# Kernel tuning notes

Measured on AMD Instinct MI355X. Metric: run time of the kernel, lower is better.

## Reference

```python
import jax, jax.numpy as jnp
import numpy as np

B, L, DIM, H, HD = 1, 2048, 2048, 16, 128  # head_dim = DIM // H; RoPE pairs = HD // 2


def setup_inputs() -> dict:
    key = jax.random.key(0)
    ks = jax.random.split(key, 6)
    x = jax.random.normal(ks[0], (B, L, DIM), dtype=jnp.float32)
    pe = jax.random.normal(ks[1], (1, 1, L, HD // 2, 2, 2), dtype=jnp.float32)
    qkv_w = jax.random.normal(ks[2], (3 * DIM, DIM), dtype=jnp.float32) * 0.02
    q_scale = jnp.ones((HD,), dtype=jnp.float32)
    k_scale = jnp.ones((HD,), dtype=jnp.float32)
    proj_w = jax.random.normal(ks[3], (DIM, DIM), dtype=jnp.float32) * 0.02
    proj_b = jnp.zeros((DIM,), dtype=jnp.float32)
    return {"x": x, "pe": pe, "qkv_w": qkv_w, "q_scale": q_scale,
            "k_scale": k_scale, "proj_w": proj_w, "proj_b": proj_b}


def _rmsnorm(t, scale):
    # per-head-dim RMSNorm, eps=1e-6, computed in fp32 (inputs already fp32)
    rrms = jax.lax.rsqrt(jnp.mean(t * t, axis=-1, keepdims=True) + 1e-6)
    return t * rrms * scale


def _apply_rope(q, k, pe):
    def rot(t):
        t_ = t.reshape(*t.shape[:-1], -1, 1, 2)  # [B,H,L,HD/2,1,2]
        out = pe[..., 0] * t_[..., 0] + pe[..., 1] * t_[..., 1]  # [B,H,L,HD/2,2]
        return out.reshape(t.shape)
    return rot(q), rot(k)


def reference(x, pe, qkv_w, q_scale, k_scale, proj_w, proj_b):
    b, l, _ = x.shape
    qkv = jnp.einsum('bld,ed->ble', x, qkv_w)  # [B, L, 3*DIM]
    qkv = qkv.reshape(b, l, 3, H, HD)
    # 'B L (K H D) -> K B H L D'
    qkv = jnp.transpose(qkv, (2, 0, 3, 1, 4))
    q, k, v = qkv[0], qkv[1], qkv[2]  # each [B, H, L, HD]
    q = _rmsnorm(q, q_scale)
    k = _rmsnorm(k, k_scale)
    q, k = _apply_rope(q, k, pe)
    scale = 1.0 / jnp.sqrt(jnp.asarray(HD, dtype=q.dtype))
    scores = jnp.einsum('bhqd,bhkd->bhqk', q, k) * scale
    attn = jax.nn.softmax(scores, axis=-1)
    out = jnp.einsum('bhqk,bhkd->bhqd', attn, v)  # [B, H, L, HD]
    out = jnp.transpose(out, (0, 2, 1, 3)).reshape(b, l, H * HD)  # 'B H L D -> B L (H D)'
    return jnp.einsum('bld,ed->ble', out, proj_w) + proj_b
```

## Files before the change

kernel.cpp:

```cpp
#include <hip/hip_runtime.h>
#include <hip/hip_bf16.h>
#include <math.h>

#define L_SEQ 2048
#define DIM   2048
#define NH    16
#define HD    128
#define TDIM  6144

typedef __attribute__((ext_vector_type(8))) short short8;
typedef __attribute__((ext_vector_type(4))) float f32x4;
typedef __attribute__((ext_vector_type(4))) unsigned int u32x4;

__device__ __forceinline__ void gl_lds16(const void* g, void* l) {
  __builtin_amdgcn_global_load_lds(
      (const __attribute__((address_space(1))) unsigned int*)g,
      (__attribute__((address_space(3))) unsigned int*)l, 16, 0, 0);
}

__device__ __forceinline__ short bf16bits(float x) {
  __hip_bfloat16 h = __float2bfloat16(x);
  return *(short*)&h;
}

__device__ __forceinline__ float bits2f(short s) {
  unsigned int u = ((unsigned int)(unsigned short)s) << 16;
  return __uint_as_float(u);
}

__device__ __forceinline__ unsigned int pack_bf16(float a, float b) {
  __hip_bfloat162 h = __float22bfloat162_rn(make_float2(a, b));
  return *(unsigned int*)&h;
}

__global__ __launch_bounds__(256)
void cast2_bf16(const float* __restrict__ a, __hip_bfloat16* __restrict__ oa,
                const float* __restrict__ b, __hip_bfloat16* __restrict__ ob) {
  int i = (blockIdx.x * 256 + threadIdx.x) * 8;
  const float* src;
  __hip_bfloat16* dst;
  int off;
  if (i < DIM * DIM) { src = a; dst = oa; off = i; }
  else               { src = b; dst = ob; off = i - DIM * DIM; }
  float4 v0 = *(const float4*)(src + off);
  float4 v1 = *(const float4*)(src + off + 4);
  short8 o;
  o[0] = bf16bits(v0.x); o[1] = bf16bits(v0.y); o[2] = bf16bits(v0.z); o[3] = bf16bits(v0.w);
  o[4] = bf16bits(v1.x); o[5] = bf16bits(v1.y); o[6] = bf16bits(v1.z); o[7] = bf16bits(v1.w);
  *(short8*)(dst + off) = o;
}

__global__ __launch_bounds__(256)
void cast_bf16(const float* __restrict__ in, __hip_bfloat16* __restrict__ out, int n) {
  int i = (blockIdx.x * 256 + threadIdx.x) * 8;
  if (i >= n) return;
  float4 a = *(const float4*)(in + i);
  float4 b = *(const float4*)(in + i + 4);
  short8 o;
  o[0] = bf16bits(a.x); o[1] = bf16bits(a.y); o[2] = bf16bits(a.z); o[3] = bf16bits(a.w);
  o[4] = bf16bits(b.x); o[5] = bf16bits(b.y); o[6] = bf16bits(b.z); o[7] = bf16bits(b.w);
  *(short8*)(out + i) = o;
}

template<int OUT_MODE>
__global__ __launch_bounds__(256)
void gemm_mfma(const __hip_bfloat16* __restrict__ A, const __hip_bfloat16* __restrict__ B,
               const float* __restrict__ bias, void* __restrict__ Cout,
               int M, int N, int K) {
  const int n0 = blockIdx.x * 128, m0 = blockIdx.y * 128;
  const int t = threadIdx.x, lane = t & 63, w = t >> 6;
  const int l15 = lane & 15, quad = lane >> 4;
  const int wm = (w & 1) * 64, wn = (w >> 1) * 64;

  __shared__ __align__(16) __hip_bfloat16 As[128 * 32];
  __shared__ __align__(16) __hip_bfloat16 Bs[128 * 32];

  f32x4 acc[4][4];
#pragma unroll
  for (int mt = 0; mt < 4; ++mt)
#pragma unroll
    for (int nt = 0; nt < 4; ++nt) acc[mt][nt] = (f32x4){0.f, 0.f, 0.f, 0.f};

  const int arow  = lane >> 2;
  const int acol8 = (lane & 3) * 8;
  const __hip_bfloat16* Ab = A + (size_t)(m0 + w * 16 + arow) * K + acol8;
  const __hip_bfloat16* Bb = B + (size_t)(n0 + w * 16 + arow) * K + acol8;
  __hip_bfloat16* As_base = As + (size_t)(w * 16) * 32;
  __hip_bfloat16* Bs_base = Bs + (size_t)(w * 16) * 32;

  for (int kb = 0; kb < K; kb += 32) {
    gl_lds16(Ab + kb,                As_base);
    gl_lds16(Ab + kb + (size_t)64*K, As_base + 64 * 32);
    gl_lds16(Bb + kb,                Bs_base);
    gl_lds16(Bb + kb + (size_t)64*K, Bs_base + 64 * 32);
    __syncthreads();

    short8 am[4], bn[4];
#pragma unroll
    for (int mt = 0; mt < 4; ++mt)
      am[mt] = *(const short8*)&As[(size_t)(wm + mt*16 + l15) * 32 + quad * 8];
#pragma unroll
    for (int nt = 0; nt < 4; ++nt)
      bn[nt] = *(const short8*)&Bs[(size_t)(wn + nt*16 + l15) * 32 + quad * 8];
#pragma unroll
    for (int mt = 0; mt < 4; ++mt)
#pragma unroll
      for (int nt = 0; nt < 4; ++nt)
        acc[mt][nt] = __builtin_amdgcn_mfma_f32_16x16x32_bf16(am[mt], bn[nt], acc[mt][nt], 0, 0, 0);
    __syncthreads();
  }

#pragma unroll
  for (int mt = 0; mt < 4; ++mt) {
#pragma unroll
    for (int nt = 0; nt < 4; ++nt) {
      int col = n0 + wn + nt * 16 + l15;
#pragma unroll
      for (int r = 0; r < 4; ++r) {
        int row = m0 + wm + mt * 16 + quad * 4 + r;
        if (OUT_MODE == 0) {
          ((__hip_bfloat16*)Cout)[(size_t)row * N + col] = __float2bfloat16(acc[mt][nt][r]);
        } else {
          ((float*)Cout)[(size_t)row * N + col] = acc[mt][nt][r] + bias[col];
        }
      }
    }
  }
}

__global__ __launch_bounds__(128)
void norm_rope(const __hip_bfloat16* __restrict__ qkv_b, const float* __restrict__ pe,
               const float* __restrict__ q_scale, const float* __restrict__ k_scale,
               __hip_bfloat16* __restrict__ Qb, __hip_bfloat16* __restrict__ Kb) {
  const int l  = blockIdx.x;
  const int hh = blockIdx.y;
  const int qk_sel = hh >> 4;
  const int h  = hh & 15;
  const int d  = threadIdx.x;
  const __hip_bfloat16* row = qkv_b + (size_t)l * TDIM + qk_sel * DIM + h * HD;
  const float* scale = qk_sel ? k_scale : q_scale;

  float v  = __bfloat162float(row[d]);
  float sq = v * v;
#pragma unroll
  for (int o = 32; o > 0; o >>= 1) sq += __shfl_xor(sq, o);
  __shared__ float wsum[2];
  if ((d & 63) == 0) wsum[d >> 6] = sq;
  __syncthreads();
  float rrms = rsqrtf((wsum[0] + wsum[1]) * (1.f / 128.f) + 1e-6f);
  __shared__ float nb[128];
  nb[d] = v * rrms * scale[d];
  __syncthreads();
  int i = d >> 1, c = d & 1;
  const float* p = pe + ((size_t)(l * 64 + i) * 2 + c) * 2;
  float res = p[0] * nb[2*i] + p[1] * nb[2*i + 1];
  size_t o_idx = ((size_t)h * L_SEQ + l) * HD + d;
  if (qk_sel == 0) Qb[o_idx] = __float2bfloat16(res * 0.08838834764831845f);
  else             Kb[o_idx] = __float2bfloat16(res);
}

__global__ __launch_bounds__(256)
void v_transpose(const __hip_bfloat16* __restrict__ qkv_b, __hip_bfloat16* __restrict__ Vt) {
  const int l0 = blockIdx.x * 64;
  const int h  = blockIdx.y;
  const int t  = threadIdx.x;
  __shared__ __align__(16) __hip_bfloat16 T[128][72];
#pragma unroll
  for (int it = 0; it < 4; ++it) {
    int idx = t + it * 256;
    int row = idx >> 4;
    int c8  = (idx & 15) * 8;
    short8 v = *(const short8*)&qkv_b[(size_t)(l0 + row) * TDIM + 2 * DIM + h * HD + c8];
#pragma unroll
    for (int j = 0; j < 8; ++j) *(short*)&T[c8 + j][row] = v[j];
  }
  __syncthreads();
#pragma unroll
  for (int it = 0; it < 4; ++it) {
    int idx = t + it * 256;
    int d = idx >> 3, c8 = (idx & 7) * 8;
    *(short8*)(Vt + ((size_t)h * HD + d) * L_SEQ + l0 + c8) = *(const short8*)&T[d][c8];
  }
}

__global__ __launch_bounds__(256, 4)
void attn_mfma(const __hip_bfloat16* __restrict__ Qb,
               const __hip_bfloat16* __restrict__ Kb,
               const __hip_bfloat16* __restrict__ Vt,
               __hip_bfloat16* __restrict__ Opart, float2* __restrict__ ml) {
  const int q0 = blockIdx.x * 64;
  const int h  = blockIdx.y;
  const int z  = blockIdx.z;
  const int t  = threadIdx.x;
  const int lane = t & 63, w = t >> 6;
  const int l15 = lane & 15, quad = lane >> 4;
  const int sw = l15 & 7;

  __shared__ __align__(16) __hip_bfloat16 Ks[64 * 128];
  __shared__ __align__(16) __hip_bfloat16 Vs[128 * 64];

  const __hip_bfloat16* kbase = Kb + (size_t)h * L_SEQ * HD;
  const __hip_bfloat16* vbase = Vt + (size_t)h * HD * L_SEQ;

  short8 aq[4];
  {
    const __hip_bfloat16* qbase = Qb + ((size_t)h * L_SEQ + q0 + w * 16 + l15) * HD;
#pragma unroll
    for (int ks = 0; ks < 4; ++ks)
      aq[ks] = *(const short8*)(qbase + ks * 32 + quad * 8);
  }

  f32x4 o[8];
#pragma unroll
  for (int n2 = 0; n2 < 8; ++n2) o[n2] = (f32x4){0.f, 0.f, 0.f, 0.f};
  float m_run = -1e30f, l_run = 0.f;

  for (int kt = 0; kt < 16; ++kt) {
    const int k0 = z * (L_SEQ / 2) + kt * 64;
#pragma unroll
    for (int i = 0; i < 4; ++i) {
      int krow = w * 16 + i * 4 + (lane >> 4);
      int kch  = (lane & 15) ^ (krow & 7);
      gl_lds16(kbase + (size_t)(k0 + krow) * HD + kch * 8,
               &Ks[(w * 16 + i * 4) * 128]);
    }
#pragma unroll
    for (int i = 0; i < 4; ++i) {
      int vrow = w * 32 + i * 8 + (lane >> 3);
      int vch  = (lane & 7) ^ (vrow & 7);
      gl_lds16(vbase + (size_t)vrow * L_SEQ + k0 + vch * 8,
               &Vs[(w * 32 + i * 8) * 64]);
    }
    __syncthreads();

    f32x4 s[4];
#pragma unroll
    for (int nt = 0; nt < 4; ++nt) s[nt] = (f32x4){0.f, 0.f, 0.f, 0.f};
#pragma unroll
    for (int ks = 0; ks < 4; ++ks) {
      short8 bk[4];
#pragma unroll
      for (int nt = 0; nt < 4; ++nt)
        bk[nt] = *(const short8*)&Ks[(nt * 16 + l15) * 128 + ((ks * 4 + quad) ^ sw) * 8];
#pragma unroll
      for (int nt = 0; nt < 4; ++nt)
        s[nt] = __builtin_amdgcn_mfma_f32_16x16x32_bf16(bk[nt], aq[ks], s[nt], 0, 0, 0);
    }

    float mx0 = fmaxf(fmaxf(s[0][0], s[0][1]), fmaxf(s[0][2], s[0][3]));
    float mx1 = fmaxf(fmaxf(s[1][0], s[1][1]), fmaxf(s[1][2], s[1][3]));
    float mx2 = fmaxf(fmaxf(s[2][0], s[2][1]), fmaxf(s[2][2], s[2][3]));
    float mx3 = fmaxf(fmaxf(s[3][0], s[3][1]), fmaxf(s[3][2], s[3][3]));
    float rm = fmaxf(fmaxf(mx0, mx1), fmaxf(mx2, mx3));
    rm = fmaxf(rm, __shfl_xor(rm, 16));
    rm = fmaxf(rm, __shfl_xor(rm, 32));
    float mnew = fmaxf(m_run, rm);
    float alpha = __expf(m_run - mnew);
    m_run = mnew;

    float sum = 0.f;
#pragma unroll
    for (int nt = 0; nt < 4; ++nt)
#pragma unroll
      for (int r = 0; r < 4; ++r) {
        float p = __expf(s[nt][r] - mnew);
        s[nt][r] = p;
        sum += p;
      }
    sum += __shfl_xor(sum, 16);
    sum += __shfl_xor(sum, 32);
    l_run = l_run * alpha + sum;

    float alpha_r[4];
#pragma unroll
    for (int r = 0; r < 4; ++r) alpha_r[r] = __shfl(alpha, quad * 4 + r);
#pragma unroll
    for (int n2 = 0; n2 < 8; ++n2)
#pragma unroll
      for (int r = 0; r < 4; ++r) o[n2][r] *= alpha_r[r];

    unsigned int pk[4][2];
#pragma unroll
    for (int nt = 0; nt < 4; ++nt) {
      pk[nt][0] = pack_bf16(s[nt][0], s[nt][1]);
      pk[nt][1] = pack_bf16(s[nt][2], s[nt][3]);
    }
    short8 ap[2];
#pragma unroll
    for (int ks2 = 0; ks2 < 2; ++ks2) {
      u32x4 a32;
#pragma unroll
      for (int jp = 0; jp < 4; ++jp) {
        int quad_src = (quad & 1) * 2 + (jp >> 1);
        int src = (quad_src << 4) | l15;
        int rp = jp & 1;
        unsigned int v0 = __shfl((int)pk[2 * ks2 + 0][rp], src);
        unsigned int v1 = __shfl((int)pk[2 * ks2 + 1][rp], src);
        a32[jp] = (quad >> 1) ? v1 : v0;
      }
      ap[ks2] = *(short8*)&a32;
    }

#pragma unroll
    for (int ks2 = 0; ks2 < 2; ++ks2)
#pragma unroll
      for (int n2 = 0; n2 < 8; ++n2) {
        short8 bv = *(const short8*)&Vs[(n2 * 16 + l15) * 64 + ((ks2 * 4 + quad) ^ sw) * 8];
        o[n2] = __builtin_amdgcn_mfma_f32_16x16x32_bf16(ap[ks2], bv, o[n2], 0, 0, 0);
      }

    __syncthreads();
  }

  const size_t rb = (size_t)(z * NH + h) * L_SEQ + q0 + w * 16;
  float linv[4];
#pragma unroll
  for (int r = 0; r < 4; ++r) linv[r] = 1.f / __shfl(l_run, quad * 4 + r);
#pragma unroll
  for (int r = 0; r < 4; ++r) {
    size_t row = rb + quad * 4 + r;
#pragma unroll
    for (int n2 = 0; n2 < 8; ++n2)
      Opart[row * HD + n2 * 16 + l15] = __float2bfloat16(o[n2][r] * linv[r]);
  }
  if (quad == 0) ml[rb + l15] = make_float2(m_run, l_run);
}

__global__ __launch_bounds__(256)
void attn_combine(const __hip_bfloat16* __restrict__ Opart,
                  const float2* __restrict__ ml,
                  __hip_bfloat16* __restrict__ out) {
  const int h  = blockIdx.y;
  const int q  = blockIdx.x * 16 + (threadIdx.x >> 4);
  const int d8 = (threadIdx.x & 15) * 8;
  const size_t i0 = (size_t)h * L_SEQ + q;
  const size_t i1 = (size_t)(NH + h) * L_SEQ + q;
  float2 a = ml[i0], b = ml[i1];
  float M  = fmaxf(a.x, b.x);
  float w1 = __expf(a.x - M) * a.y;
  float w2 = __expf(b.x - M) * b.y;
  float inv = 1.f / (w1 + w2);
  w1 *= inv; w2 *= inv;
  short8 o1 = *(const short8*)&Opart[i0 * HD + d8];
  short8 o2 = *(const short8*)&Opart[i1 * HD + d8];
  short8 r;
#pragma unroll
  for (int j = 0; j < 8; ++j)
    r[j] = bf16bits(w1 * bits2f(o1[j]) + w2 * bits2f(o2[j]));
  *(short8*)&out[(size_t)q * DIM + h * HD + d8] = r;
}

extern "C" void kernel_launch(void* const* d_in, const int* in_sizes, int n_in,
                              void* d_out, int out_size, void* d_ws, size_t ws_size,
                              hipStream_t stream) {
  const float* x       = (const float*)d_in[0];
  const float* pe      = (const float*)d_in[1];
  const float* qkv_w   = (const float*)d_in[2];
  const float* q_scale = (const float*)d_in[3];
  const float* k_scale = (const float*)d_in[4];
  const float* proj_w  = (const float*)d_in[5];
  const float* proj_b  = (const float*)d_in[6];
  float* out = (float*)d_out;

  char* base = (char*)d_ws;
  __hip_bfloat16* wb       = (__hip_bfloat16*)base;
  __hip_bfloat16* qkv_b    = (__hip_bfloat16*)(base + 25165824);
  __hip_bfloat16* xb       = (__hip_bfloat16*)(base + 50331648);
  __hip_bfloat16* Qb       = (__hip_bfloat16*)base;
  __hip_bfloat16* Kb       = (__hip_bfloat16*)(base + 8388608);
  __hip_bfloat16* Vt       = (__hip_bfloat16*)(base + 16777216);
  __hip_bfloat16* pwb      = (__hip_bfloat16*)(base + 25165824);
  __hip_bfloat16* Opart    = (__hip_bfloat16*)(base + 33554432);
  float2*         ml       = (float2*)(base + 50331648);
  __hip_bfloat16* attn_out = (__hip_bfloat16*)base;

  cast2_bf16<<<dim3((DIM * DIM + TDIM * DIM) / (256 * 8)), 256, 0, stream>>>(
      x, xb, qkv_w, wb);

  gemm_mfma<0><<<dim3(TDIM / 128, L_SEQ / 128), 256, 0, stream>>>(
      xb, wb, nullptr, qkv_b, L_SEQ, TDIM, DIM);

  norm_rope<<<dim3(L_SEQ, 2 * NH), 128, 0, stream>>>(qkv_b, pe, q_scale, k_scale, Qb, Kb);
  v_transpose<<<dim3(L_SEQ / 64, NH), 256, 0, stream>>>(qkv_b, Vt);

  cast_bf16<<<dim3(DIM * DIM / (256 * 8)), 256, 0, stream>>>(proj_w, pwb, DIM * DIM);

  attn_mfma<<<dim3(L_SEQ / 64, NH, 2), 256, 0, stream>>>(Qb, Kb, Vt, Opart, ml);
  attn_combine<<<dim3(L_SEQ / 16, NH), 256, 0, stream>>>(Opart, ml, attn_out);

  gemm_mfma<1><<<dim3(DIM / 128, DIM / 128), 256, 0, stream>>>(
      attn_out, pwb, proj_b, out, L_SEQ, DIM, DIM);
}
```

Measured before the change: 343.0 us.

## Fuse RMSNorm, RoPE and V transpose into the QKV GEMM epilogue

The QKV GEMM epilogue now stages each 128x128 output tile in shared memory. For Q and K column tiles it applies per-head RMSNorm, RoPE and the softmax scale, then writes the head-major Qb and Kb directly. For V tiles it writes the transposed Vt layout. This drops the qkv_b intermediate round trip through global memory and two kernel launches, at the cost of a larger shared-memory footprint and a heavier GEMM epilogue. Workspace offsets are reshuffled so the buffers do not alias.

```diff
diff --git a/kernel.cpp b/kernel.cpp
--- a/kernel.cpp
+++ b/kernel.cpp
@@ -62,18 +62,22 @@
   *(short8*)(out + i) = o;
 }
 
-template<int OUT_MODE>
 __global__ __launch_bounds__(256)
-void gemm_mfma(const __hip_bfloat16* __restrict__ A, const __hip_bfloat16* __restrict__ B,
-               const float* __restrict__ bias, void* __restrict__ Cout,
-               int M, int N, int K) {
-  const int n0 = blockIdx.x * 128, m0 = blockIdx.y * 128;
+void gemm_qkv_fused(const __hip_bfloat16* __restrict__ A, const __hip_bfloat16* __restrict__ B,
+                    const float* __restrict__ q_scale, const float* __restrict__ k_scale,
+                    const float* __restrict__ pe,
+                    __hip_bfloat16* __restrict__ Qb, __hip_bfloat16* __restrict__ Kb,
+                    __hip_bfloat16* __restrict__ Vt) {
+  const int K = DIM;
+  const int bx = blockIdx.x;
+  const int n0 = bx * 128, m0 = blockIdx.y * 128;
   const int t = threadIdx.x, lane = t & 63, w = t >> 6;
   const int l15 = lane & 15, quad = lane >> 4;
   const int wm = (w & 1) * 64, wn = (w >> 1) * 64;
 
-  __shared__ __align__(16) __hip_bfloat16 As[128 * 32];
-  __shared__ __align__(16) __hip_bfloat16 Bs[128 * 32];
+  __shared__ __align__(16) char smem[128 * 136 * 2];
+  __hip_bfloat16* As = (__hip_bfloat16*)smem;
+  __hip_bfloat16* Bs = As + 128 * 32;
 
   f32x4 acc[4][4];
 #pragma unroll
@@ -110,77 +114,142 @@
     __syncthreads();
   }
 
-#pragma unroll
-  for (int mt = 0; mt < 4; ++mt) {
+  __hip_bfloat16* T = (__hip_bfloat16*)smem;
+
+  if (bx < 32) {
+    const float* scale = (bx < 16) ? q_scale : k_scale;
+    const float qmul = (bx < 16) ? 0.08838834764831845f : 1.0f;
+    __hip_bfloat16* dst = (bx < 16) ? Qb : Kb;
+    const int h = bx & 15;
+
+#pragma unroll
+    for (int mt = 0; mt < 4; ++mt)
+#pragma unroll
+      for (int nt = 0; nt < 4; ++nt) {
+        int d = wn + nt * 16 + l15;
+#pragma unroll
+        for (int r = 0; r < 4; ++r)
+          T[(wm + mt * 16 + quad * 4 + r) * 136 + d] = __float2bfloat16(acc[mt][nt][r]);
+      }
+    __syncthreads();
+
+    const int row  = t >> 1;
+    const int half = t & 1;
+    const __hip_bfloat16* Trow = T + row * 136 + half * 64;
+
+    float ss = 0.f;
+#pragma unroll
+    for (int c8 = 0; c8 < 64; c8 += 8) {
+      short8 v8 = *(const short8*)(Trow + c8);
+#pragma unroll
+      for (int j = 0; j < 8; ++j) { float f = bits2f(v8[j]); ss += f * f; }
+    }
+    ss += __shfl_xor(ss, 1);
+    const float rrms = rsqrtf(ss * (1.f / 128.f) + 1e-6f);
+
+    const int l = m0 + row;
+    const float* perow = pe + (size_t)l * 256 + half * 128;
+    __hip_bfloat16* drow = dst + ((size_t)h * L_SEQ + l) * HD + half * 64;
+
+#pragma unroll
+    for (int c8 = 0; c8 < 64; c8 += 8) {
+      short8 v8 = *(const short8*)(Trow + c8);
+      float f[8];
+#pragma unroll
+      for (int j = 0; j < 8; ++j)
+        f[j] = bits2f(v8[j]) * rrms * scale[half * 64 + c8 + j];
+      short8 o;
+#pragma unroll
+      for (int p = 0; p < 4; ++p) {
+        float4 pp = *(const float4*)(perow + c8 * 2 + p * 4);
+        float e = f[2 * p], od = f[2 * p + 1];
+        o[2 * p]     = bf16bits((pp.x * e + pp.y * od) * qmul);
+        o[2 * p + 1] = bf16bits((pp.z * e + pp.w * od) * qmul);
+      }
+      *(short8*)(drow + c8) = o;
+    }
+  } else {
+    const int h = bx - 32;
+#pragma unroll
+    for (int mt = 0; mt < 4; ++mt)
+#pragma unroll
+      for (int nt = 0; nt < 4; ++nt) {
+        int d = wn + nt * 16 + l15;
+#pragma unroll
+        for (int r = 0; r < 4; ++r) {
+          int l_local = wm + mt * 16 + quad * 4 + r;
+          T[d * 136 + l_local] = __float2bfloat16(acc[mt][nt][r]);
+        }
+      }
+    __syncthreads();
+#pragma unroll
+    for (int it = 0; it < 8; ++it) {
+      int idx = t + it * 256;
+      int d = idx >> 4, c8 = (idx & 15) * 8;
+      short8 v = *(const short8*)&T[d * 136 + c8];
+      *(short8*)&Vt[((size_t)h * HD + d) * L_SEQ + m0 + c8] = v;
+    }
+  }
+}
+
+__global__ __launch_bounds__(256)
+void gemm_proj(const __hip_bfloat16* __restrict__ A, const __hip_bfloat16* __restrict__ B,
+               const float* __restrict__ bias, float* __restrict__ C,
+               int M, int N, int K) {
+  const int n0 = blockIdx.x * 128, m0 = blockIdx.y * 128;
+  const int t = threadIdx.x, lane = t & 63, w = t >> 6;
+  const int l15 = lane & 15, quad = lane >> 4;
+  const int wm = (w & 1) * 64, wn = (w >> 1) * 64;
+
+  __shared__ __align__(16) __hip_bfloat16 As[128 * 32];
+  __shared__ __align__(16) __hip_bfloat16 Bs[128 * 32];
+
+  f32x4 acc[4][4];
+#pragma unroll
+  for (int mt = 0; mt < 4; ++mt)
+#pragma unroll
+    for (int nt = 0; nt < 4; ++nt) acc[mt][nt] = (f32x4){0.f, 0.f, 0.f, 0.f};
+
+  const int arow  = lane >> 2;
+  const int acol8 = (lane & 3) * 8;
+  const __hip_bfloat16* Ab = A + (size_t)(m0 + w * 16 + arow) * K + acol8;
+  const __hip_bfloat16* Bb = B + (size_t)(n0 + w * 16 + arow) * K + acol8;
+  __hip_bfloat16* As_base = As + (size_t)(w * 16) * 32;
+  __hip_bfloat16* Bs_base = Bs + (size_t)(w * 16) * 32;
+
+  for (int kb = 0; kb < K; kb += 32) {
+    gl_lds16(Ab + kb,                As_base);
+    gl_lds16(Ab + kb + (size_t)64*K, As_base + 64 * 32);
+    gl_lds16(Bb + kb,                Bs_base);
+    gl_lds16(Bb + kb + (size_t)64*K, Bs_base + 64 * 32);
+    __syncthreads();
+
+    short8 am[4], bn[4];
+#pragma unroll
+    for (int mt = 0; mt < 4; ++mt)
+      am[mt] = *(const short8*)&As[(size_t)(wm + mt*16 + l15) * 32 + quad * 8];
+#pragma unroll
+    for (int nt = 0; nt < 4; ++nt)
+      bn[nt] = *(const short8*)&Bs[(size_t)(wn + nt*16 + l15) * 32 + quad * 8];
+#pragma unroll
+    for (int mt = 0; mt < 4; ++mt)
+#pragma unroll
+      for (int nt = 0; nt < 4; ++nt)
+        acc[mt][nt] = __builtin_amdgcn_mfma_f32_16x16x32_bf16(am[mt], bn[nt], acc[mt][nt], 0, 0, 0);
+    __syncthreads();
+  }
+
+#pragma unroll
+  for (int mt = 0; mt < 4; ++mt)
 #pragma unroll
     for (int nt = 0; nt < 4; ++nt) {
       int col = n0 + wn + nt * 16 + l15;
 #pragma unroll
       for (int r = 0; r < 4; ++r) {
         int row = m0 + wm + mt * 16 + quad * 4 + r;
-        if (OUT_MODE == 0) {
-          ((__hip_bfloat16*)Cout)[(size_t)row * N + col] = __float2bfloat16(acc[mt][nt][r]);
-        } else {
-          ((float*)Cout)[(size_t)row * N + col] = acc[mt][nt][r] + bias[col];
-        }
-      }
-    }
-  }
-}
-
-__global__ __launch_bounds__(128)
-void norm_rope(const __hip_bfloat16* __restrict__ qkv_b, const float* __restrict__ pe,
-               const float* __restrict__ q_scale, const float* __restrict__ k_scale,
-               __hip_bfloat16* __restrict__ Qb, __hip_bfloat16* __restrict__ Kb) {
-  const int l  = blockIdx.x;
-  const int hh = blockIdx.y;
-  const int qk_sel = hh >> 4;
-  const int h  = hh & 15;
-  const int d  = threadIdx.x;
-  const __hip_bfloat16* row = qkv_b + (size_t)l * TDIM + qk_sel * DIM + h * HD;
-  const float* scale = qk_sel ? k_scale : q_scale;
-
-  float v  = __bfloat162float(row[d]);
-  float sq = v * v;
-#pragma unroll
-  for (int o = 32; o > 0; o >>= 1) sq += __shfl_xor(sq, o);
-  __shared__ float wsum[2];
-  if ((d & 63) == 0) wsum[d >> 6] = sq;
-  __syncthreads();
-  float rrms = rsqrtf((wsum[0] + wsum[1]) * (1.f / 128.f) + 1e-6f);
-  __shared__ float nb[128];
-  nb[d] = v * rrms * scale[d];
-  __syncthreads();
-  int i = d >> 1, c = d & 1;
-  const float* p = pe + ((size_t)(l * 64 + i) * 2 + c) * 2;
-  float res = p[0] * nb[2*i] + p[1] * nb[2*i + 1];
-  size_t o_idx = ((size_t)h * L_SEQ + l) * HD + d;
-  if (qk_sel == 0) Qb[o_idx] = __float2bfloat16(res * 0.08838834764831845f);
-  else             Kb[o_idx] = __float2bfloat16(res);
-}
-
-__global__ __launch_bounds__(256)
-void v_transpose(const __hip_bfloat16* __restrict__ qkv_b, __hip_bfloat16* __restrict__ Vt) {
-  const int l0 = blockIdx.x * 64;
-  const int h  = blockIdx.y;
-  const int t  = threadIdx.x;
-  __shared__ __align__(16) __hip_bfloat16 T[128][72];
-#pragma unroll
-  for (int it = 0; it < 4; ++it) {
-    int idx = t + it * 256;
-    int row = idx >> 4;
-    int c8  = (idx & 15) * 8;
-    short8 v = *(const short8*)&qkv_b[(size_t)(l0 + row) * TDIM + 2 * DIM + h * HD + c8];
-#pragma unroll
-    for (int j = 0; j < 8; ++j) *(short*)&T[c8 + j][row] = v[j];
-  }
-  __syncthreads();
-#pragma unroll
-  for (int it = 0; it < 4; ++it) {
-    int idx = t + it * 256;
-    int d = idx >> 3, c8 = (idx & 7) * 8;
-    *(short8*)(Vt + ((size_t)h * HD + d) * L_SEQ + l0 + c8) = *(const short8*)&T[d][c8];
-  }
+        C[(size_t)row * N + col] = acc[mt][nt][r] + bias[col];
+      }
+    }
 }
 
 __global__ __launch_bounds__(256, 4)
@@ -363,31 +432,27 @@
   float* out = (float*)d_out;
 
   char* base = (char*)d_ws;
-  __hip_bfloat16* wb       = (__hip_bfloat16*)base;
-  __hip_bfloat16* qkv_b    = (__hip_bfloat16*)(base + 25165824);
-  __hip_bfloat16* xb       = (__hip_bfloat16*)(base + 50331648);
-  __hip_bfloat16* Qb       = (__hip_bfloat16*)base;
-  __hip_bfloat16* Kb       = (__hip_bfloat16*)(base + 8388608);
-  __hip_bfloat16* Vt       = (__hip_bfloat16*)(base + 16777216);
-  __hip_bfloat16* pwb      = (__hip_bfloat16*)(base + 25165824);
-  __hip_bfloat16* Opart    = (__hip_bfloat16*)(base + 33554432);
-  float2*         ml       = (float2*)(base + 50331648);
+  __hip_bfloat16* xb       = (__hip_bfloat16*)base;
+  __hip_bfloat16* wb       = (__hip_bfloat16*)(base + 8388608);
+  __hip_bfloat16* Qb       = (__hip_bfloat16*)(base + 33554432);
+  __hip_bfloat16* Kb       = (__hip_bfloat16*)(base + 41943040);
+  __hip_bfloat16* Vt       = (__hip_bfloat16*)(base + 50331648);
+  __hip_bfloat16* pwb      = (__hip_bfloat16*)(base + 58720256);
+  __hip_bfloat16* Opart    = (__hip_bfloat16*)(base + 8388608);
+  float2*         ml       = (float2*)(base + 25165824);
   __hip_bfloat16* attn_out = (__hip_bfloat16*)base;
 
   cast2_bf16<<<dim3((DIM * DIM + TDIM * DIM) / (256 * 8)), 256, 0, stream>>>(
       x, xb, qkv_w, wb);
 
-  gemm_mfma<0><<<dim3(TDIM / 128, L_SEQ / 128), 256, 0, stream>>>(
-      xb, wb, nullptr, qkv_b, L_SEQ, TDIM, DIM);
-
-  norm_rope<<<dim3(L_SEQ, 2 * NH), 128, 0, stream>>>(qkv_b, pe, q_scale, k_scale, Qb, Kb);
-  v_transpose<<<dim3(L_SEQ / 64, NH), 256, 0, stream>>>(qkv_b, Vt);
+  gemm_qkv_fused<<<dim3(TDIM / 128, L_SEQ / 128), 256, 0, stream>>>(
+      xb, wb, q_scale, k_scale, pe, Qb, Kb, Vt);
 
   cast_bf16<<<dim3(DIM * DIM / (256 * 8)), 256, 0, stream>>>(proj_w, pwb, DIM * DIM);
 
   attn_mfma<<<dim3(L_SEQ / 64, NH, 2), 256, 0, stream>>>(Qb, Kb, Vt, Opart, ml);
   attn_combine<<<dim3(L_SEQ / 16, NH), 256, 0, stream>>>(Opart, ml, attn_out);
 
-  gemm_mfma<1><<<dim3(DIM / 128, DIM / 128), 256, 0, stream>>>(
+  gemm_proj<<<dim3(DIM / 128, DIM / 128), 256, 0, stream>>>(
       attn_out, pwb, proj_b, out, L_SEQ, DIM, DIM);
 }
```

Result: no change. 340.7 us (-0.6%).
